# Kernel tuning notes

Hardware: AMD Instinct MI355X
Metric: run time of the kernel (lower is better)

The kernel has to match this reference:

```python
import jax, jax.numpy as jnp
import numpy as np

B, T, D, H = 4, 4096, 1024, 16
CAP = 0.5


def setup_inputs() -> dict:
    key = jax.random.key(0)
    ks = jax.random.split(key, 8)
    s = 0.02
    n = lambda k, shape: jax.random.normal(k, shape, dtype=jnp.float32) * s
    return {
        "x": jax.random.normal(ks[0], (B, T, D), dtype=jnp.float32),
        "w_router": n(ks[1], (D,)),
        "in_proj_w": n(ks[2], (3 * D, D)),
        "in_proj_b": jnp.zeros((3 * D,), jnp.float32),
        "out_proj_w": n(ks[3], (D, D)),
        "out_proj_b": jnp.zeros((D,), jnp.float32),
        "w1": n(ks[4], (4 * D, D)),
        "b1": jnp.zeros((4 * D,), jnp.float32),
        "w2": n(ks[5], (D, 4 * D)),
        "b2": jnp.zeros((D,), jnp.float32),
        "ln1_g": jnp.ones((D,), jnp.float32),
        "ln1_b": jnp.zeros((D,), jnp.float32),
        "ln2_g": jnp.ones((D,), jnp.float32),
        "ln2_b": jnp.zeros((D,), jnp.float32),
    }


def _ln(x, g, b, eps=1e-5):
    mu = jnp.mean(x, -1, keepdims=True)
    var = jnp.var(x, -1, keepdims=True)  # population variance, matches torch LayerNorm
    return (x - mu) * jax.lax.rsqrt(var + eps) * g + b


def reference(x, w_router, in_proj_w, in_proj_b, out_proj_w, out_proj_b,
              w1, b1, w2, b2, ln1_g, ln1_b, ln2_g, ln2_b):
    Bx, Tx, Dx = x.shape
    k = max(1, int(Tx * CAP))  # tokens routed through the block, same k for every batch row
    logits = x @ w_router  # (B,T) scalar router scores
    aux = jnp.mean(logits ** 2) * 0.01
    # top-k selection; sort indices ascending = boolean-mask gather order in torch
    idx = jnp.sort(jax.lax.top_k(logits, k)[1], axis=-1)  # (B,k)
    xs = jnp.take_along_axis(x, idx[:, :, None], axis=1)  # (B,k,D)

    h = _ln(xs, ln1_g, ln1_b)
    qkv = h @ in_proj_w.T + in_proj_b  # (B,k,3D)
    q, kk, v = jnp.split(qkv, 3, axis=-1)
    dh = Dx // H
    heads = lambda t: t.reshape(Bx, k, H, dh).transpose(0, 2, 1, 3)  # (B,H,k,dh)
    q, kk, v = heads(q), heads(kk), heads(v)
    scores = jnp.einsum('bhqd,bhkd->bhqk', q, kk) / jnp.sqrt(jnp.float32(dh))
    attn = jax.nn.softmax(scores, axis=-1)
    o = jnp.einsum('bhqk,bhkd->bhqd', attn, v).transpose(0, 2, 1, 3).reshape(Bx, k, Dx)
    o = o @ out_proj_w.T + out_proj_b
    xs = xs + o
    h2 = _ln(xs, ln2_g, ln2_b)
    ff = jax.nn.gelu(h2 @ w1.T + b1, approximate=False) @ w2.T + b2
    xs = xs + ff
    # scatter processed tokens back; unselected tokens pass through unchanged
    out = x.at[jnp.arange(Bx)[:, None], idx].set(xs)
    return out, aux
```

## Files before the change

kernel.cpp:

```cpp
#include <hip/hip_runtime.h>

#define B_    4
#define T_    4096
#define D_    1024
#define H_    16
#define DH_   64
#define KTOK  2048
#define MROWS (B_*KTOK)

typedef unsigned short u16;
typedef __attribute__((ext_vector_type(8))) short short8;
typedef __attribute__((ext_vector_type(4))) float f32x4;
typedef __attribute__((ext_vector_type(4))) unsigned int u32x4;
typedef __attribute__((ext_vector_type(2))) unsigned int u32x2;
typedef __attribute__((ext_vector_type(4))) unsigned short u16x4;

static __device__ __forceinline__ u16 f2bf(float f) {
  union { float f; unsigned int u; } a; a.f = f;
  unsigned int u = a.u;
  unsigned int r = (u + 0x7FFFu + ((u >> 16) & 1u)) >> 16;
  return (u16)r;
}

#if defined(__has_builtin)
#if __has_builtin(__builtin_amdgcn_exp2f)
#define EXP2F(x) __builtin_amdgcn_exp2f(x)
#endif
#endif
#ifndef EXP2F
#define EXP2F(x) exp2f(x)
#endif

static __device__ __forceinline__ float gelu_f(float v) {
  float x = fabsf(v) * 0.70710678118654752f;
  float t = __builtin_amdgcn_rcpf(1.0f + 0.3275911f * x);
  float p = t * (0.254829592f + t * (-0.284496736f + t * (1.421413741f +
            t * (-1.453152027f + t * 1.061405429f))));
  float e = EXP2F(-1.4426950408889634f * x * x);
  float er = 1.0f - p * e;
  er = (v < 0.0f) ? -er : er;
  return 0.5f * v * (1.0f + er);
}

static __device__ __forceinline__ unsigned int pkbf_t(float a, float b) {
  unsigned int ua = __builtin_bit_cast(unsigned int, a);
  unsigned int ub = __builtin_bit_cast(unsigned int, b);
  return __builtin_amdgcn_perm(ub, ua, 0x07060302u);
}

static __device__ __forceinline__ void gld_lds16(const u16* g, u16* l) {
  __builtin_amdgcn_global_load_lds((__attribute__((address_space(1))) void*)g,
                                   (__attribute__((address_space(3))) void*)l, 16, 0, 0);
}

#define WAITV(N) asm volatile("s_waitcnt vmcnt(" #N ")" ::: "memory")

__global__ void __launch_bounds__(256) router_kernel(const float* __restrict__ x,
    const float* __restrict__ wr, float* __restrict__ logits, float* __restrict__ auxacc)
{
  int tid = threadIdx.x; int lane = tid & 63, wave = tid >> 6;
  int row = blockIdx.x * 4 + wave;
  const float* xr = x + (size_t)row * D_;
  float dot = 0.f;
#pragma unroll
  for (int j = 0; j < 4; j++) {
    int c = j * 256 + lane * 4;
    f32x4 xv = *(const f32x4*)(xr + c);
    f32x4 wv = *(const f32x4*)(wr + c);
    dot += xv[0]*wv[0] + xv[1]*wv[1] + xv[2]*wv[2] + xv[3]*wv[3];
  }
#pragma unroll
  for (int d = 1; d < 64; d <<= 1) dot += __shfl_xor(dot, d);
  __shared__ float red[4];
  if (lane == 0) { logits[row] = dot; red[wave] = dot; }
  __syncthreads();
  if (tid == 0) {
    float a = red[0]*red[0] + red[1]*red[1] + red[2]*red[2] + red[3]*red[3];
    atomicAdd(auxacc, a);
  }
}

__global__ void __launch_bounds__(256) rankp_kernel(const float* __restrict__ logits,
    int* __restrict__ rnk)
{
  __shared__ float ll[256];
  const int b = blockIdx.y, ch = blockIdx.z;
  const int tid = threadIdx.x;
  const float* lg = logits + (size_t)b * T_;
  const int j0 = ch * 256;
  ll[tid] = lg[j0 + tid];
  __syncthreads();
  const int t = blockIdx.x * 256 + tid;
  const float my = lg[t];
  int rank = 0;
#pragma unroll 4
  for (int j = 0; j < 256; j += 4) {
    f32x4 lj = *(const f32x4*)&ll[j];
    int jg = j0 + j;
    rank += (lj[0] > my) || (lj[0] == my && (jg+0) < t);
    rank += (lj[1] > my) || (lj[1] == my && (jg+1) < t);
    rank += (lj[2] > my) || (lj[2] == my && (jg+2) < t);
    rank += (lj[3] > my) || (lj[3] == my && (jg+3) < t);
  }
  atomicAdd(&rnk[(size_t)b * T_ + t], rank);
}

__global__ void __launch_bounds__(256) lnpass_kernel(const float* __restrict__ x,
    const int* __restrict__ rnk, const float* __restrict__ g, const float* __restrict__ bb,
    float* __restrict__ xs_out, u16* __restrict__ hout, float* __restrict__ out,
    int* __restrict__ idx, const float* __restrict__ acc, float* __restrict__ auxout)
{
  int row = blockIdx.x;
  int tid = threadIdx.x;
  if (row == 0 && tid == 0) auxout[0] = acc[0] * (0.01f / (float)(B_ * T_));
  const float* srow = x + (size_t)row * D_;
  f32x4 v = *(const f32x4*)(srow + tid * 4);
  int r = rnk[row];
  if (r >= KTOK) {
    *(f32x4*)(out + (size_t)row * D_ + tid * 4) = v;
    return;
  }
  if (tid == 0) idx[(row >> 12) * KTOK + r] = row & (T_ - 1);
  size_t mrow = (size_t)(row >> 12) * KTOK + r;
  float s  = v[0] + v[1] + v[2] + v[3];
  float sq = v[0]*v[0] + v[1]*v[1] + v[2]*v[2] + v[3]*v[3];
#pragma unroll
  for (int d = 1; d < 64; d <<= 1) { s += __shfl_xor(s, d); sq += __shfl_xor(sq, d); }
  __shared__ float rs[4], rq[4];
  int lane = tid & 63, wave = tid >> 6;
  if (lane == 0) { rs[wave] = s; rq[wave] = sq; }
  __syncthreads();
  s  = rs[0] + rs[1] + rs[2] + rs[3];
  sq = rq[0] + rq[1] + rq[2] + rq[3];
  float mean = s * (1.0f / D_);
  float var  = sq * (1.0f / D_) - mean * mean;
  float rstd = rsqrtf(var + 1e-5f);
  f32x4 gg = *(const f32x4*)(g + tid * 4);
  f32x4 bv = *(const f32x4*)(bb + tid * 4);
  *(f32x4*)(xs_out + mrow * D_ + tid * 4) = v;
  u16x4 o;
#pragma unroll
  for (int j = 0; j < 4; j++) o[j] = f2bf((v[j] - mean) * rstd * gg[j] + bv[j]);
  *(u16x4*)(hout + mrow * D_ + tid * 4) = o;
}

__global__ void __launch_bounds__(256) ln2_kernel(const float* __restrict__ src,
    const float* __restrict__ g, const float* __restrict__ bb, u16* __restrict__ hout)
{
  int row = blockIdx.x;
  int tid = threadIdx.x;
  const float* srow = src + (size_t)row * D_;
  f32x4 v = *(const f32x4*)(srow + tid * 4);
  float s  = v[0] + v[1] + v[2] + v[3];
  float sq = v[0]*v[0] + v[1]*v[1] + v[2]*v[2] + v[3]*v[3];
#pragma unroll
  for (int d = 1; d < 64; d <<= 1) { s += __shfl_xor(s, d); sq += __shfl_xor(sq, d); }
  __shared__ float rs[4], rq[4];
  int lane = tid & 63, wave = tid >> 6;
  if (lane == 0) { rs[wave] = s; rq[wave] = sq; }
  __syncthreads();
  s  = rs[0] + rs[1] + rs[2] + rs[3];
  sq = rq[0] + rq[1] + rq[2] + rq[3];
  float mean = s * (1.0f / D_);
  float var  = sq * (1.0f / D_) - mean * mean;
  float rstd = rsqrtf(var + 1e-5f);
  f32x4 gg = *(const f32x4*)(g + tid * 4);
  f32x4 bv = *(const f32x4*)(bb + tid * 4);
  u16x4 o;
#pragma unroll
  for (int j = 0; j < 4; j++) o[j] = f2bf((v[j] - mean) * rstd * gg[j] + bv[j]);
  *(u16x4*)(hout + (size_t)row * D_ + tid * 4) = o;
}

__global__ void __launch_bounds__(256) f2bf_all(const float* __restrict__ s0, const float* __restrict__ s1,
    const float* __restrict__ s2, const float* __restrict__ s3,
    u16* __restrict__ d0, u16* __restrict__ d1, u16* __restrict__ d2, u16* __restrict__ d3)
{
  const size_t c0 = (size_t)3 * D_ * D_, c1 = (size_t)4 * D_ * D_, c2 = (size_t)8 * D_ * D_;
  size_t e = (size_t)blockIdx.x * 1024 + (size_t)threadIdx.x * 4;
  const float* s; u16* d; size_t off;
  if (e < c0)      { s = s0; d = d0; off = e; }
  else if (e < c1) { s = s1; d = d1; off = e - c0; }
  else if (e < c2) { s = s2; d = d2; off = e - c1; }
  else             { s = s3; d = d3; off = e - c2; }
  f32x4 v = *(const f32x4*)(s + off);
  u16x4 o; o[0]=f2bf(v[0]); o[1]=f2bf(v[1]); o[2]=f2bf(v[2]); o[3]=f2bf(v[3]);
  *(u16x4*)(d + off) = o;
}

template<int EPI, bool AHM = false>
__global__ void __launch_bounds__(256, 2) gemm_bt(
    const u16* __restrict__ A, const u16* __restrict__ W,
    const float* __restrict__ bias, float* __restrict__ xs,
    u16* __restrict__ Cb, float* __restrict__ outf,
    const int* __restrict__ idx, u16* __restrict__ vtb, int M, int N, int K)
{
  __shared__ u16 As[2][128 * 64];
  __shared__ u16 Ws[2][128 * 64];
  const int tid = threadIdx.x;
  const int lane = tid & 63, wave = tid >> 6;
  const int m16 = lane & 15, quad = (lane >> 4) & 3;

  const int gx = gridDim.x;
  const int id = blockIdx.y * gx + blockIdx.x;
  const int cpx = (gx * (int)gridDim.y) >> 3;
  const int tl = (id & 7) * cpx + (id >> 3);
  const int bx = tl % gx, by = tl / gx;

  const size_t arow0 = (size_t)by * 128;
  const size_t wrow0 = (size_t)bx * 128;

  const int trow = tid >> 3;
  const int tcc  = (tid ^ trow) & 7;
  auto stagepc = [&](const u16* g0, size_t rs, u16* l0) {
    gld_lds16(g0 + (size_t)trow * rs + tcc * 8,        l0 + (size_t)(tid & ~63) * 8);
    gld_lds16(g0 + (size_t)(32 + trow) * rs + tcc * 8, l0 + 2048 + (size_t)(tid & ~63) * 8);
  };
  auto stage_tile = [&](int u, int s) {
    size_t kn = (size_t)u * 64;
    if (AHM) {
      const u16* Ab = A + (arow0 >> 11) * (size_t)(H_ * KTOK * DH_)
                        + (arow0 & (KTOK - 1)) * DH_ + (size_t)u * (KTOK * DH_);
      stagepc(Ab,            64, &As[s][0]);
      stagepc(Ab + 64 * 64,  64, &As[s][64 * 64]);
    } else {
      stagepc(A + (arow0)      * K + kn, K, &As[s][0]);
      stagepc(A + (arow0 + 64) * K + kn, K, &As[s][64 * 64]);
    }
    stagepc(W + (wrow0)      * K + kn, K, &Ws[s][0]);
    stagepc(W + (wrow0 + 64) * K + kn, K, &Ws[s][64 * 64]);
  };

  auto ldA = [&](short8 (&f)[2][2], const u16* h) {
#pragma unroll
    for (int mt = 0; mt < 2; mt++) {
      int rr = wave * 32 + mt * 16 + m16;
      int sw = rr & 7;
#pragma unroll
      for (int kk = 0; kk < 2; kk++)
        f[mt][kk] = *(const short8*)&h[rr * 64 + (((kk * 4 + quad) ^ sw) * 8)];
    }
  };
  auto ldB = [&](short8 (&f)[4][2], const u16* h, int half) {
#pragma unroll
    for (int nt = 0; nt < 4; nt++) {
      int rb = half * 64 + nt * 16 + m16;
      int sw = rb & 7;
#pragma unroll
      for (int kk = 0; kk < 2; kk++)
        f[nt][kk] = *(const short8*)&h[rb * 64 + (((kk * 4 + quad) ^ sw) * 8)];
    }
  };

  f32x4 acc[2][8];
#pragma unroll
  for (int mt = 0; mt < 2; mt++)
#pragma unroll
    for (int n = 0; n < 8; n++) acc[mt][n] = (f32x4)0.0f;

  stage_tile(0, 0);

  const int NT = K >> 6;
  short8 af[2][2], bf[4][2], bf2[4][2];

  for (int t = 0; t < NT; t++) {
    const int cur = t & 1;
    const bool last = (t == NT - 1);

    WAITV(2);
    __builtin_amdgcn_s_barrier();
    __builtin_amdgcn_sched_barrier(0);
    if (!last) stage_tile(t + 1, cur ^ 1);

    ldA(af, &As[cur][0]);
    ldB(bf, &Ws[cur][0], 0);
    __builtin_amdgcn_s_setprio(1);
#pragma unroll
    for (int mt = 0; mt < 2; mt++)
#pragma unroll
      for (int nt = 0; nt < 4; nt++)
#pragma unroll
        for (int kk = 0; kk < 2; kk++)
          acc[mt][nt] = __builtin_amdgcn_mfma_f32_16x16x32_bf16(af[mt][kk], bf[nt][kk], acc[mt][nt], 0, 0, 0);
    __builtin_amdgcn_s_setprio(0);

    if (last) { WAITV(0); } else { WAITV(8); }
    __builtin_amdgcn_s_barrier();
    __builtin_amdgcn_sched_barrier(0);

    ldB(bf2, &Ws[cur][0], 1);
    __builtin_amdgcn_s_setprio(1);
#pragma unroll
    for (int mt = 0; mt < 2; mt++)
#pragma unroll
      for (int nt = 0; nt < 4; nt++)
#pragma unroll
        for (int kk = 0; kk < 2; kk++)
          acc[mt][4 + nt] = __builtin_amdgcn_mfma_f32_16x16x32_bf16(af[mt][kk], bf2[nt][kk], acc[mt][4 + nt], 0, 0, 0);
    __builtin_amdgcn_s_setprio(0);
  }

#pragma unroll
  for (int half = 0; half < 2; half++) {
#pragma unroll
    for (int mt = 0; mt < 2; mt++) {
#pragma unroll
      for (int nt = 0; nt < 4; nt++) {
        f32x4 a = acc[mt][half * 4 + nt];
        size_t col = wrow0 + half * 64 + nt * 16 + m16;
        float bvv = bias[col];
        size_t rowb = arow0 + wave * 32 + mt * 16 + quad * 4;
        if (EPI == 0) {
          if ((int)col < 2 * D_) {
            float sc = ((int)col < D_) ? 0.18033688f : 1.0f;
#pragma unroll
            for (int r = 0; r < 4; r++)
              Cb[(rowb + r) * (size_t)N + col] = f2bf((a[r] + bvv) * sc);
          } else {
            int hdh = (int)col - 2 * D_;
            int bb2 = (int)(rowb >> 11);
            int tok = (int)(rowb & (KTOK - 1));
            u16x4 o;
#pragma unroll
            for (int r = 0; r < 4; r++) o[r] = f2bf(a[r] + bvv);
            *(u16x4*)&vtb[(((size_t)(bb2 * H_) + (hdh >> 6)) * 64 + (hdh & 63)) * KTOK + tok] = o;
          }
        } else if (EPI == 1) {
#pragma unroll
          for (int r = 0; r < 4; r++) {
            size_t o = (rowb + r) * (size_t)N + col;
            xs[o] = xs[o] + (a[r] + bvv);
          }
        } else {
#pragma unroll
          for (int r = 0; r < 4; r++) {
            size_t row = rowb + r;
            int b = (int)(row >> 11);
            int i = (int)(row & (KTOK - 1));
            int t = idx[b * KTOK + i];
            float vv = xs[row * (size_t)D_ + col] + (a[r] + bvv);
            outf[((size_t)b * T_ + t) * D_ + col] = vv;
          }
        }
      }
    }
  }
}

__global__ void __launch_bounds__(512, 1) gemm_ff1(
    const u16* __restrict__ A, const u16* __restrict__ W,
    const float* __restrict__ bias, u16* __restrict__ Cb, int M, int N, int K)
{
  __shared__ u16 Asm[2][2][128 * 64];
  __shared__ u16 Bsm[2][2][128 * 64];

  const int tid = threadIdx.x;
  const int lane = tid & 63;
  const int w = tid >> 6;
  const int m16 = lane & 15, quad = (lane >> 4) & 3;
  const int rowA = (w >> 2) * 64;
  const int rowB = (w & 3) * 32;

  const int gx = gridDim.x;
  const int id = blockIdx.y * gx + blockIdx.x;
  const int cpx = (gx * (int)gridDim.y) >> 3;
  const int tl = (id & 7) * cpx + (id >> 3);
  const int bx = tl % gx, by = tl / gx;

  const int arow0 = by * 256;
  const int wcol0 = bx * 256;

  const int th8 = tid >> 3;
  const int ccs = (tid ^ th8) & 7;
  auto stage = [&](const u16* g0, u16* l0) {
    gld_lds16(g0 + (size_t)th8 * K + ccs * 8,        l0 + (size_t)(tid & ~63) * 8);
    gld_lds16(g0 + (size_t)(64 + th8) * K + ccs * 8, l0 + 4096 + (size_t)(tid & ~63) * 8);
  };
  auto stage_tile = [&](int u, int s) {
    size_t kn = (size_t)u * 64;
    stage(A + (size_t)arow0 * K + kn,         &Asm[s][0][0]);
    stage(W + (size_t)wcol0 * K + kn,         &Bsm[s][0][0]);
    stage(A + (size_t)(arow0 + 128) * K + kn, &Asm[s][1][0]);
    stage(W + (size_t)(wcol0 + 128) * K + kn, &Bsm[s][1][0]);
  };

  auto ldA = [&](short8 (&f)[4][2], const u16* h) {
#pragma unroll
    for (int mt = 0; mt < 4; mt++) {
      int rr = rowA + mt * 16 + m16;
      int sw = rr & 7;
#pragma unroll
      for (int kk = 0; kk < 2; kk++)
        f[mt][kk] = *(const short8*)&h[rr * 64 + (((kk * 4 + quad) ^ sw) * 8)];
    }
  };
  auto ldB = [&](short8 (&f)[2][2], const u16* h) {
#pragma unroll
    for (int nt = 0; nt < 2; nt++) {
      int rb = rowB + nt * 16 + m16;
      int sw = rb & 7;
#pragma unroll
      for (int kk = 0; kk < 2; kk++)
        f[nt][kk] = *(const short8*)&h[rb * 64 + (((kk * 4 + quad) ^ sw) * 8)];
    }
  };

  f32x4 acc[4][4][2];
#pragma unroll
  for (int q = 0; q < 4; q++)
#pragma unroll
    for (int mt = 0; mt < 4; mt++)
#pragma unroll
      for (int nt = 0; nt < 2; nt++) acc[q][mt][nt] = (f32x4)0.0f;

#define MMQ(QD, FA, FB) do { \
  __builtin_amdgcn_s_setprio(1); \
  _Pragma("unroll") for (int mt = 0; mt < 4; mt++) \
  _Pragma("unroll") for (int nt = 0; nt < 2; nt++) \
  _Pragma("unroll") for (int kk = 0; kk < 2; kk++) \
    acc[QD][mt][nt] = __builtin_amdgcn_mfma_f32_16x16x32_bf16(FA[mt][kk], FB[nt][kk], acc[QD][mt][nt], 0, 0, 0); \
  __builtin_amdgcn_s_setprio(0); } while (0)

  stage_tile(0, 0);

  const int NT = K >> 6;
  short8 af[4][2], af2[4][2], bf[2][2], bf2[2][2];

  for (int t = 0; t < NT; t++) {
    const int cur = t & 1;
    const bool last = (t == NT - 1);

    WAITV(4);
    __builtin_amdgcn_s_barrier();
    __builtin_amdgcn_sched_barrier(0);
    if (!last) stage_tile(t + 1, cur ^ 1);

    ldA(af, &Asm[cur][0][0]);
    ldB(bf, &Bsm[cur][0][0]);
    MMQ(0, af, bf);

    if (last) { WAITV(0); } else { WAITV(8); }
    __builtin_amdgcn_s_barrier();
    __builtin_amdgcn_sched_barrier(0);

    ldB(bf2, &Bsm[cur][1][0]);
    MMQ(1, af, bf2);
    ldA(af2, &Asm[cur][1][0]);
    MMQ(2, af2, bf);
    MMQ(3, af2, bf2);
  }
#undef MMQ

#pragma unroll
  for (int qd = 0; qd < 4; qd++) {
    const int ha = qd >> 1, hb = qd & 1;
#pragma unroll
    for (int mt = 0; mt < 4; mt++) {
#pragma unroll
      for (int nt = 0; nt < 2; nt++) {
        f32x4 a = acc[qd][mt][nt];
        size_t col = (size_t)wcol0 + hb * 128 + (w & 3) * 32 + nt * 16 + m16;
        float bvv = bias[col];
        size_t rowb = (size_t)arow0 + ha * 128 + (w >> 2) * 64 + mt * 16 + quad * 4;
#pragma unroll
        for (int r = 0; r < 4; r++)
          Cb[(rowb + r) * (size_t)N + col] = f2bf(gelu_f(a[r] + bvv));
      }
    }
  }
}

__global__ void __launch_bounds__(512, 2) attn_kernel(const u16* __restrict__ qkv,
                                                      const u16* __restrict__ vtb,
                                                      u16* __restrict__ obuf)
{
  __shared__ u16 Ks[3][64 * 64];
  __shared__ u16 Vs[3][64 * 64];
  __shared__ u16 Ps[8][2][16 * 64];

  const int tid = threadIdx.x;
  const int lane = tid & 63, wave = tid >> 6;
  const int m16 = lane & 15, quad = lane >> 4;
  const int bh = blockIdx.x;
  const int b = bh >> 4, h = bh & 15;
  const int q0 = blockIdx.y * 256 + wave * 32;

  const u16* base = qkv + ((size_t)b * KTOK) * (3 * D_) + h * DH_;
  const u16* vb   = vtb + (size_t)bh * 64 * KTOK;

  short8 qf[2][2];
#pragma unroll
  for (int qh = 0; qh < 2; qh++) {
    const u16* qrow = base + (size_t)(q0 + qh * 16 + m16) * (3 * D_);
    qf[qh][0] = *(const short8*)(qrow + quad * 8);
    qf[qh][1] = *(const short8*)(qrow + 32 + quad * 8);
  }
  short8 vone;
#pragma unroll
  for (int i = 0; i < 8; i++) vone[i] = (short)0x3F80;

  f32x4 oacc[2][4];
#pragma unroll
  for (int qh = 0; qh < 2; qh++)
#pragma unroll
    for (int nt = 0; nt < 4; nt++) oacc[qh][nt] = (f32x4)0.0f;
  f32x4 lacc[2] = {(f32x4)0.0f, (f32x4)0.0f};

  auto stage_kv = [&](int u, int s) {
    int key = tid >> 3;
    int cc = (tid ^ key) & 7;
    gld_lds16(base + (size_t)(u * 64 + key) * (3 * D_) + D_ + cc * 8,
              &Ks[s][0] + (size_t)(tid & ~63) * 8);
    gld_lds16(vb + (u * 64) + (size_t)key * KTOK + cc * 8,
              &Vs[s][0] + (size_t)(tid & ~63) * 8);
  };

  const int NT = KTOK / 64;
  stage_kv(0, 0);
  stage_kv(1, 1);
  WAITV(2);
  __builtin_amdgcn_s_barrier();
  __builtin_amdgcn_sched_barrier(0);

  const int sw = m16 & 7;
  int buf = 0;
  for (int t = 0; t < NT; t++) {
    if (t + 2 < NT) {
      int s2 = buf + 2; if (s2 >= 3) s2 -= 3;
      stage_kv(t + 2, s2);
    }
    const u16* Kb = &Ks[buf][0];
    const u16* Vb = &Vs[buf][0];

    f32x4 sacc[2][4];
#pragma unroll
    for (int qh = 0; qh < 2; qh++)
#pragma unroll
      for (int nt = 0; nt < 4; nt++) sacc[qh][nt] = (f32x4)0.0f;
    __builtin_amdgcn_s_setprio(1);
#pragma unroll
    for (int nt = 0; nt < 4; nt++) {
      int row = nt * 16 + m16;
      int ksw = row & 7;
      short8 kf0 = *(const short8*)&Kb[row * 64 + ((quad ^ ksw) * 8)];
      short8 kf1 = *(const short8*)&Kb[row * 64 + (((4 + quad) ^ ksw) * 8)];
#pragma unroll
      for (int qh = 0; qh < 2; qh++) {
        sacc[qh][nt] = __builtin_amdgcn_mfma_f32_16x16x32_bf16(kf0, qf[qh][0], sacc[qh][nt], 0, 0, 0);
        sacc[qh][nt] = __builtin_amdgcn_mfma_f32_16x16x32_bf16(kf1, qf[qh][1], sacc[qh][nt], 0, 0, 0);
      }
    }
    __builtin_amdgcn_s_setprio(0);

    short8 vf[4][2];
#pragma unroll
    for (int nt = 0; nt < 4; nt++) {
      int row = nt * 16 + m16;
      int vsw = row & 7;
      vf[nt][0] = *(const short8*)&Vb[row * 64 + ((quad ^ vsw) * 8)];
      vf[nt][1] = *(const short8*)&Vb[row * 64 + (((4 + quad) ^ vsw) * 8)];
    }

#pragma unroll
    for (int qh = 0; qh < 2; qh++) {
#pragma unroll
      for (int nt = 0; nt < 4; nt++) {
        f32x4 p;
#pragma unroll
        for (int r = 0; r < 4; r++) p[r] = EXP2F(sacc[qh][nt][r]);
        u32x2 w2; w2[0] = pkbf_t(p[0], p[1]); w2[1] = pkbf_t(p[2], p[3]);
        int c16 = 2 * nt + (quad >> 1);
        *(u32x2*)&Ps[wave][qh][m16 * 64 + ((c16 ^ sw) * 8) + (quad & 1) * 4] = w2;
      }
    }
    short8 pa[2][2];
#pragma unroll
    for (int qh = 0; qh < 2; qh++) {
      pa[qh][0] = *(const short8*)&Ps[wave][qh][m16 * 64 + ((quad ^ sw) * 8)];
      pa[qh][1] = *(const short8*)&Ps[wave][qh][m16 * 64 + (((4 + quad) ^ sw) * 8)];
    }
    __builtin_amdgcn_s_setprio(1);
#pragma unroll
    for (int qh = 0; qh < 2; qh++) {
#pragma unroll
      for (int nt = 0; nt < 4; nt++) {
        oacc[qh][nt] = __builtin_amdgcn_mfma_f32_16x16x32_bf16(pa[qh][0], vf[nt][0], oacc[qh][nt], 0, 0, 0);
        oacc[qh][nt] = __builtin_amdgcn_mfma_f32_16x16x32_bf16(pa[qh][1], vf[nt][1], oacc[qh][nt], 0, 0, 0);
      }
      lacc[qh] = __builtin_amdgcn_mfma_f32_16x16x32_bf16(pa[qh][0], vone, lacc[qh], 0, 0, 0);
      lacc[qh] = __builtin_amdgcn_mfma_f32_16x16x32_bf16(pa[qh][1], vone, lacc[qh], 0, 0, 0);
    }
    __builtin_amdgcn_s_setprio(0);

    if (t < NT - 1) {
      if (t < NT - 2) { WAITV(2); } else { WAITV(0); }
      __builtin_amdgcn_s_barrier();
      __builtin_amdgcn_sched_barrier(0);
    }
    buf = (buf == 2) ? 0 : buf + 1;
  }

#pragma unroll
  for (int qh = 0; qh < 2; qh++) {
    f32x4 rl;
#pragma unroll
    for (int r = 0; r < 4; r++) rl[r] = 1.0f / lacc[qh][r];
#pragma unroll
    for (int nt = 0; nt < 4; nt++)
#pragma unroll
      for (int r = 0; r < 4; r++) {
        int qq = q0 + qh * 16 + quad * 4 + r;
        float v = oacc[qh][nt][r] * rl[r];
        obuf[((size_t)bh * KTOK + qq) * DH_ + nt * 16 + m16] = f2bf(v);
      }
  }
}

extern "C" void kernel_launch(void* const* d_in, const int* in_sizes, int n_in,
                              void* d_out, int out_size, void* d_ws, size_t ws_size,
                              hipStream_t stream)
{
  (void)in_sizes; (void)n_in; (void)out_size; (void)ws_size;
  const float* x          = (const float*)d_in[0];
  const float* w_router   = (const float*)d_in[1];
  const float* in_proj_w  = (const float*)d_in[2];
  const float* in_proj_b  = (const float*)d_in[3];
  const float* out_proj_w = (const float*)d_in[4];
  const float* out_proj_b = (const float*)d_in[5];
  const float* w1         = (const float*)d_in[6];
  const float* b1         = (const float*)d_in[7];
  const float* w2         = (const float*)d_in[8];
  const float* b2         = (const float*)d_in[9];
  const float* ln1g       = (const float*)d_in[10];
  const float* ln1b       = (const float*)d_in[11];
  const float* ln2g       = (const float*)d_in[12];
  const float* ln2b       = (const float*)d_in[13];
  float* out = (float*)d_out;

  char* w = (char*)d_ws;
  auto alloc = [&](size_t bytes) -> char* {
    char* p = w; w += (bytes + 255) & ~(size_t)255; return p;
  };
  float* logits = (float*)alloc((size_t)B_ * T_ * 4);
  int*   rnk    = (int*)  alloc((size_t)B_ * T_ * 4);
  int*   idx    = (int*)  alloc((size_t)B_ * KTOK * 4);
  float* auxacc = (float*)alloc(256);
  u16* inpw  = (u16*)alloc((size_t)3 * D_ * D_ * 2);
  u16* outpw = (u16*)alloc((size_t)D_ * D_ * 2);
  u16* w1b   = (u16*)alloc((size_t)4 * D_ * D_ * 2);
  u16* w2b   = (u16*)alloc((size_t)4 * D_ * D_ * 2);
  float* xs  = (float*)alloc((size_t)MROWS * D_ * 4);
  u16* hbuf  = (u16*)alloc((size_t)MROWS * D_ * 2);
  char* region = alloc((size_t)MROWS * 4 * D_ * 2);
  u16* qkvb = (u16*)region;
  u16* obuf = (u16*)(region + (size_t)MROWS * 3 * D_ * 2);
  u16* ffb  = (u16*)region;
  u16* vtb  = (u16*)alloc((size_t)B_ * H_ * DH_ * KTOK * 2);

  (void)hipMemsetAsync(auxacc, 0, 4, stream);
  (void)hipMemsetAsync(rnk, 0, (size_t)B_ * T_ * 4, stream);

  router_kernel<<<B_ * T_ / 4, 256, 0, stream>>>(x, w_router, logits, auxacc);
  rankp_kernel<<<dim3(T_ / 256, B_, 16), 256, 0, stream>>>(logits, rnk);
  lnpass_kernel<<<B_ * T_, 256, 0, stream>>>(x, rnk, ln1g, ln1b, xs, hbuf, out,
                                             idx, auxacc, out + (size_t)B_ * T_ * D_);

  f2bf_all<<<12 * D_ * D_ / 1024, 256, 0, stream>>>(in_proj_w, out_proj_w, w1, w2,
                                                    inpw, outpw, w1b, w2b);

  gemm_bt<0><<<dim3(3 * D_ / 128, MROWS / 128), 256, 0, stream>>>(
      hbuf, inpw, in_proj_b, nullptr, qkvb, nullptr, nullptr, vtb, MROWS, 3 * D_, D_);
  attn_kernel<<<dim3(B_ * H_, KTOK / 256), 512, 0, stream>>>(qkvb, vtb, obuf);
  gemm_bt<1, true><<<dim3(D_ / 128, MROWS / 128), 256, 0, stream>>>(
      obuf, outpw, out_proj_b, xs, nullptr, nullptr, nullptr, nullptr, MROWS, D_, D_);
  ln2_kernel<<<MROWS, 256, 0, stream>>>(xs, ln2g, ln2b, hbuf);
  gemm_ff1<<<dim3(4 * D_ / 256, MROWS / 256), 512, 0, stream>>>(
      hbuf, w1b, b1, ffb, MROWS, 4 * D_, D_);
  gemm_bt<3><<<dim3(D_ / 128, MROWS / 128), 256, 0, stream>>>(
      ffb, w2b, b2, xs, nullptr, out, idx, nullptr, MROWS, D_, 4 * D_);
}
```

Measured before the change: 634.8 us.

## Use 32x32x16 MFMA in attention and keep P in registers via permlane32 swap

Rewrites the attention inner loop to use 32x32x16 bf16 MFMAs instead of 16x16x32. The exp'd score tile is repacked into the A-operand layout with v_permlane32_swap, so the per-wave LDS round-trip through the Ps buffer is gone. This removes LDS writes and reads per tile and cuts the number of MFMA issues. It relies on the layout of the permlane32 swap being correct, and the larger accumulators raise register pressure under launch_bounds(512,2). The attention kernel is only part of the total pipeline time.

```diff
diff --git a/kernel.cpp b/kernel.cpp
--- a/kernel.cpp
+++ b/kernel.cpp
@@ -11,6 +11,7 @@
 typedef unsigned short u16;
 typedef __attribute__((ext_vector_type(8))) short short8;
 typedef __attribute__((ext_vector_type(4))) float f32x4;
+typedef __attribute__((ext_vector_type(16))) float f32x16;
 typedef __attribute__((ext_vector_type(4))) unsigned int u32x4;
 typedef __attribute__((ext_vector_type(2))) unsigned int u32x2;
 typedef __attribute__((ext_vector_type(4))) unsigned short u16x4;
@@ -46,6 +47,10 @@
   unsigned int ua = __builtin_bit_cast(unsigned int, a);
   unsigned int ub = __builtin_bit_cast(unsigned int, b);
   return __builtin_amdgcn_perm(ub, ua, 0x07060302u);
+}
+
+static __device__ __forceinline__ void pl32swap(unsigned int &a, unsigned int &b) {
+  asm volatile("v_permlane32_swap_b32 %0, %1" : "+v"(a), "+v"(b));
 }
 
 static __device__ __forceinline__ void gld_lds16(const u16* g, u16* l) {
@@ -476,11 +481,10 @@
 {
   __shared__ u16 Ks[3][64 * 64];
   __shared__ u16 Vs[3][64 * 64];
-  __shared__ u16 Ps[8][2][16 * 64];
 
   const int tid = threadIdx.x;
   const int lane = tid & 63, wave = tid >> 6;
-  const int m16 = lane & 15, quad = lane >> 4;
+  const int l31 = lane & 31, hi = lane >> 5;
   const int bh = blockIdx.x;
   const int b = bh >> 4, h = bh & 15;
   const int q0 = blockIdx.y * 256 + wave * 32;
@@ -488,23 +492,20 @@
   const u16* base = qkv + ((size_t)b * KTOK) * (3 * D_) + h * DH_;
   const u16* vb   = vtb + (size_t)bh * 64 * KTOK;
 
-  short8 qf[2][2];
-#pragma unroll
-  for (int qh = 0; qh < 2; qh++) {
-    const u16* qrow = base + (size_t)(q0 + qh * 16 + m16) * (3 * D_);
-    qf[qh][0] = *(const short8*)(qrow + quad * 8);
-    qf[qh][1] = *(const short8*)(qrow + 32 + quad * 8);
+  short8 qf[4];
+  {
+    const u16* qrow = base + (size_t)(q0 + l31) * (3 * D_);
+#pragma unroll
+    for (int ks = 0; ks < 4; ks++)
+      qf[ks] = *(const short8*)(qrow + ks * 16 + hi * 8);
   }
   short8 vone;
 #pragma unroll
   for (int i = 0; i < 8; i++) vone[i] = (short)0x3F80;
 
-  f32x4 oacc[2][4];
-#pragma unroll
-  for (int qh = 0; qh < 2; qh++)
-#pragma unroll
-    for (int nt = 0; nt < 4; nt++) oacc[qh][nt] = (f32x4)0.0f;
-  f32x4 lacc[2] = {(f32x4)0.0f, (f32x4)0.0f};
+  f32x16 oacc[2];
+  oacc[0] = (f32x16)0.0f; oacc[1] = (f32x16)0.0f;
+  f32x16 lacc = (f32x16)0.0f;
 
   auto stage_kv = [&](int u, int s) {
     int key = tid >> 3;
@@ -522,7 +523,6 @@
   __builtin_amdgcn_s_barrier();
   __builtin_amdgcn_sched_barrier(0);
 
-  const int sw = m16 & 7;
   int buf = 0;
   for (int t = 0; t < NT; t++) {
     if (t + 2 < NT) {
@@ -532,64 +532,51 @@
     const u16* Kb = &Ks[buf][0];
     const u16* Vb = &Vs[buf][0];
 
-    f32x4 sacc[2][4];
-#pragma unroll
-    for (int qh = 0; qh < 2; qh++)
-#pragma unroll
-      for (int nt = 0; nt < 4; nt++) sacc[qh][nt] = (f32x4)0.0f;
+    unsigned int w[2][8];
+#pragma unroll
+    for (int kg = 0; kg < 2; kg++) {
+      f32x16 sacc = (f32x16)0.0f;
+      __builtin_amdgcn_s_setprio(1);
+#pragma unroll
+      for (int ks = 0; ks < 4; ks++) {
+        int row = kg * 32 + l31;
+        int c = (ks * 2 + hi) ^ (row & 7);
+        short8 kf = *(const short8*)&Kb[row * 64 + c * 8];
+        sacc = __builtin_amdgcn_mfma_f32_32x32x16_bf16(kf, qf[ks], sacc, 0, 0, 0);
+      }
+      __builtin_amdgcn_s_setprio(0);
+#pragma unroll
+      for (int i = 0; i < 8; i++) {
+        float p0 = EXP2F(sacc[2 * i]);
+        float p1 = EXP2F(sacc[2 * i + 1]);
+        w[kg][i] = pkbf_t(p0, p1);
+      }
+      pl32swap(w[kg][0], w[kg][2]); pl32swap(w[kg][1], w[kg][3]);
+      pl32swap(w[kg][4], w[kg][6]); pl32swap(w[kg][5], w[kg][7]);
+    }
+    short8 pa[4];
+#pragma unroll
+    for (int kg = 0; kg < 2; kg++)
+#pragma unroll
+      for (int kk = 0; kk < 2; kk++) {
+        u32x4 d; d[0] = w[kg][kk*4]; d[1] = w[kg][kk*4+1]; d[2] = w[kg][kk*4+2]; d[3] = w[kg][kk*4+3];
+        pa[kg * 2 + kk] = __builtin_bit_cast(short8, d);
+      }
+
     __builtin_amdgcn_s_setprio(1);
 #pragma unroll
-    for (int nt = 0; nt < 4; nt++) {
-      int row = nt * 16 + m16;
-      int ksw = row & 7;
-      short8 kf0 = *(const short8*)&Kb[row * 64 + ((quad ^ ksw) * 8)];
-      short8 kf1 = *(const short8*)&Kb[row * 64 + (((4 + quad) ^ ksw) * 8)];
-#pragma unroll
-      for (int qh = 0; qh < 2; qh++) {
-        sacc[qh][nt] = __builtin_amdgcn_mfma_f32_16x16x32_bf16(kf0, qf[qh][0], sacc[qh][nt], 0, 0, 0);
-        sacc[qh][nt] = __builtin_amdgcn_mfma_f32_16x16x32_bf16(kf1, qf[qh][1], sacc[qh][nt], 0, 0, 0);
+    for (int dg = 0; dg < 2; dg++) {
+#pragma unroll
+      for (int j = 0; j < 4; j++) {
+        int row = dg * 32 + l31;
+        int c = (j * 2 + hi) ^ (row & 7);
+        short8 vf = *(const short8*)&Vb[row * 64 + c * 8];
+        oacc[dg] = __builtin_amdgcn_mfma_f32_32x32x16_bf16(pa[j], vf, oacc[dg], 0, 0, 0);
       }
     }
-    __builtin_amdgcn_s_setprio(0);
-
-    short8 vf[4][2];
-#pragma unroll
-    for (int nt = 0; nt < 4; nt++) {
-      int row = nt * 16 + m16;
-      int vsw = row & 7;
-      vf[nt][0] = *(const short8*)&Vb[row * 64 + ((quad ^ vsw) * 8)];
-      vf[nt][1] = *(const short8*)&Vb[row * 64 + (((4 + quad) ^ vsw) * 8)];
-    }
-
-#pragma unroll
-    for (int qh = 0; qh < 2; qh++) {
-#pragma unroll
-      for (int nt = 0; nt < 4; nt++) {
-        f32x4 p;
-#pragma unroll
-        for (int r = 0; r < 4; r++) p[r] = EXP2F(sacc[qh][nt][r]);
-        u32x2 w2; w2[0] = pkbf_t(p[0], p[1]); w2[1] = pkbf_t(p[2], p[3]);
-        int c16 = 2 * nt + (quad >> 1);
-        *(u32x2*)&Ps[wave][qh][m16 * 64 + ((c16 ^ sw) * 8) + (quad & 1) * 4] = w2;
-      }
-    }
-    short8 pa[2][2];
-#pragma unroll
-    for (int qh = 0; qh < 2; qh++) {
-      pa[qh][0] = *(const short8*)&Ps[wave][qh][m16 * 64 + ((quad ^ sw) * 8)];
-      pa[qh][1] = *(const short8*)&Ps[wave][qh][m16 * 64 + (((4 + quad) ^ sw) * 8)];
-    }
-    __builtin_amdgcn_s_setprio(1);
-#pragma unroll
-    for (int qh = 0; qh < 2; qh++) {
-#pragma unroll
-      for (int nt = 0; nt < 4; nt++) {
-        oacc[qh][nt] = __builtin_amdgcn_mfma_f32_16x16x32_bf16(pa[qh][0], vf[nt][0], oacc[qh][nt], 0, 0, 0);
-        oacc[qh][nt] = __builtin_amdgcn_mfma_f32_16x16x32_bf16(pa[qh][1], vf[nt][1], oacc[qh][nt], 0, 0, 0);
-      }
-      lacc[qh] = __builtin_amdgcn_mfma_f32_16x16x32_bf16(pa[qh][0], vone, lacc[qh], 0, 0, 0);
-      lacc[qh] = __builtin_amdgcn_mfma_f32_16x16x32_bf16(pa[qh][1], vone, lacc[qh], 0, 0, 0);
-    }
+#pragma unroll
+    for (int j = 0; j < 4; j++)
+      lacc = __builtin_amdgcn_mfma_f32_32x32x16_bf16(pa[j], vone, lacc, 0, 0, 0);
     __builtin_amdgcn_s_setprio(0);
 
     if (t < NT - 1) {
@@ -601,18 +588,12 @@
   }
 
 #pragma unroll
-  for (int qh = 0; qh < 2; qh++) {
-    f32x4 rl;
-#pragma unroll
-    for (int r = 0; r < 4; r++) rl[r] = 1.0f / lacc[qh][r];
-#pragma unroll
-    for (int nt = 0; nt < 4; nt++)
-#pragma unroll
-      for (int r = 0; r < 4; r++) {
-        int qq = q0 + qh * 16 + quad * 4 + r;
-        float v = oacc[qh][nt][r] * rl[r];
-        obuf[((size_t)bh * KTOK + qq) * DH_ + nt * 16 + m16] = f2bf(v);
-      }
+  for (int r = 0; r < 16; r++) {
+    float rl = 1.0f / lacc[r];
+    int qq = q0 + (r & 3) + 8 * (r >> 2) + 4 * hi;
+#pragma unroll
+    for (int dg = 0; dg < 2; dg++)
+      obuf[((size_t)bh * KTOK + qq) * DH_ + dg * 32 + l31] = f2bf(oacc[dg][r] * rl);
   }
 }
 
```

After: 616.4 us. 2.9% less time.
